# Performance work log

Measured on AMD Instinct MI355X. Metric: run time of the kernel, lower is better.

Reference implementation:

```python
import jax, jax.numpy as jnp
import numpy as np

B, S, H = 2, 2048, 2048
NH, NKV, HD = 16, 4, 128
GROUPS = NH // NKV
THETA = 10000.0
EPS = 1e-6


def setup_inputs() -> dict:
    key = jax.random.key(0)
    ks = jax.random.split(key, 6)
    scale = 0.02
    return {
        "hidden_states": jax.random.normal(ks[0], (B, S, H), jnp.float32),
        "wq": jax.random.normal(ks[1], (NH * HD, H), jnp.float32) * scale,
        "wk": jax.random.normal(ks[2], (NKV * HD, H), jnp.float32) * scale,
        "wv": jax.random.normal(ks[3], (NKV * HD, H), jnp.float32) * scale,
        "wo": jax.random.normal(ks[4], (H, NH * HD), jnp.float32) * scale,
        "q_norm_weight": jnp.ones((HD,), jnp.float32),
        "k_norm_weight": jnp.ones((HD,), jnp.float32),
    }


def _rope_tables(seq_len):
    inv_freq = 1.0 / (THETA ** (jnp.arange(0, HD, 2, dtype=jnp.float32) / HD))
    t = jnp.arange(seq_len, dtype=jnp.float32)
    freqs = jnp.outer(t, inv_freq)              # [S, HD/2]
    emb = jnp.concatenate([freqs, freqs], -1)   # [S, HD]
    return jnp.cos(emb), jnp.sin(emb)


def _rotate_half(x):
    x1, x2 = x[..., : HD // 2], x[..., HD // 2:]
    return jnp.concatenate([-x2, x1], -1)


def _rmsnorm(x, w):
    var = jnp.mean(jnp.square(x), axis=-1, keepdims=True)
    return x * jax.lax.rsqrt(var + EPS) * w


def reference(hidden_states, wq, wk, wv, wo, q_norm_weight, k_norm_weight):
    b, s, _ = hidden_states.shape
    q = (hidden_states @ wq.T).reshape(b, s, NH, HD).transpose(0, 2, 1, 3)    # [b,nh,s,d]
    k = (hidden_states @ wk.T).reshape(b, s, NKV, HD).transpose(0, 2, 1, 3)   # [b,nkv,s,d]
    v = (hidden_states @ wv.T).reshape(b, s, NKV, HD).transpose(0, 2, 1, 3)

    cos, sin = _rope_tables(s)                  # [s,d]
    q = q * cos + _rotate_half(q) * sin
    k = k * cos + _rotate_half(k) * sin

    # fused QK RMSNorm (applied inside fused_qknorm_flash_attention)
    q = _rmsnorm(q, q_norm_weight)
    k = _rmsnorm(k, k_norm_weight)

    # GQA: share each kv head across GROUPS query heads without materializing repeats
    qg = q.reshape(b, NKV, GROUPS, s, HD)
    scale = 1.0 / jnp.sqrt(jnp.float32(HD))
    scores = jnp.einsum('bhgqd,bhkd->bhgqk', qg, k) * scale   # [b,nkv,g,s,s]
    causal = jnp.tril(jnp.ones((s, s), bool))
    scores = jnp.where(causal, scores, jnp.finfo(scores.dtype).min)
    probs = jax.nn.softmax(scores, axis=-1)
    out = jnp.einsum('bhgqk,bhkd->bhgqd', probs, v)            # [b,nkv,g,s,d]
    out = out.reshape(b, NH, s, HD).transpose(0, 2, 1, 3).reshape(b, s, NH * HD)
    return out @ wo.T
```

## Files before the change

### kernel.cpp

```cpp
#include <hip/hip_runtime.h>
#include <math.h>

typedef __bf16 bf16;
typedef __bf16 bf16x8 __attribute__((ext_vector_type(8)));
typedef __bf16 bf16x4 __attribute__((ext_vector_type(4)));
typedef float f32x4 __attribute__((ext_vector_type(4)));

#define B_DIM 2
#define S_LEN 2048
#define H_DIM 2048
#define NH 16
#define NKV 4
#define HD 128

__device__ __forceinline__ void gl_lds16(const void* g, void* l) {
    __builtin_amdgcn_global_load_lds(
        (const __attribute__((address_space(1))) unsigned int*)g,
        (__attribute__((address_space(3))) unsigned int*)l, 16, 0, 0);
}

__global__ __launch_bounds__(256) void cast_all(const float* __restrict__ s0,
                                                const float* __restrict__ s1,
                                                const float* __restrict__ s2,
                                                const float* __restrict__ s3,
                                                const float* __restrict__ s4,
                                                bf16* __restrict__ dst) {
    const int i = blockIdx.x * 256 + threadIdx.x;
    const float* src;
    int off;
    if (i < 2097152)      { src = s0; off = 0; }
    else if (i < 3145728) { src = s1; off = 2097152; }
    else if (i < 3407872) { src = s2; off = 3145728; }
    else if (i < 3670016) { src = s3; off = 3407872; }
    else                  { src = s4; off = 3670016; }
    float4 f = ((const float4*)src)[i - off];
    bf16x4 o = { (bf16)f.x, (bf16)f.y, (bf16)f.z, (bf16)f.w };
    *(bf16x4*)(dst + (size_t)i * 4) = o;
}

template <typename OutT>
__global__ __launch_bounds__(256) void gemm_bt(const bf16* __restrict__ A,
                                               const bf16* __restrict__ Bt,
                                               OutT* __restrict__ C,
                                               int M, int N, int K) {
    __shared__ __align__(16) bf16 As[128 * 32];
    __shared__ __align__(16) bf16 Bs[128 * 32];
    const int t = threadIdx.x;
    const int lane = t & 63, w = t >> 6;
    const int wm = (w & 1) * 64, wn = (w >> 1) * 64;
    const int lr = lane & 15, quad = lane >> 4;
    const int m0 = blockIdx.x * 128, n0 = blockIdx.y * 128;
    const int lrow = lane >> 2, lk = (lane & 3) * 8;
    f32x4 acc[4][4];
#pragma unroll
    for (int i = 0; i < 4; i++)
#pragma unroll
        for (int j = 0; j < 4; j++) acc[i][j] = (f32x4){0.f, 0.f, 0.f, 0.f};

    for (int k0 = 0; k0 < K; k0 += 32) {
        __syncthreads();
#pragma unroll
        for (int i = 0; i < 2; i++) {
            const int r0 = i * 64 + w * 16;
            gl_lds16(A + (size_t)(m0 + r0 + lrow) * K + k0 + lk, &As[r0 * 32]);
            gl_lds16(Bt + (size_t)(n0 + r0 + lrow) * K + k0 + lk, &Bs[r0 * 32]);
        }
        __syncthreads();
        bf16x8 af[4], bfr[4];
#pragma unroll
        for (int i = 0; i < 4; i++) af[i] = *(const bf16x8*)&As[(wm + i * 16 + lr) * 32 + quad * 8];
#pragma unroll
        for (int j = 0; j < 4; j++) bfr[j] = *(const bf16x8*)&Bs[(wn + j * 16 + lr) * 32 + quad * 8];
#pragma unroll
        for (int i = 0; i < 4; i++)
#pragma unroll
            for (int j = 0; j < 4; j++)
                acc[i][j] = __builtin_amdgcn_mfma_f32_16x16x32_bf16(af[i], bfr[j], acc[i][j], 0, 0, 0);
    }
#pragma unroll
    for (int i = 0; i < 4; i++) {
        int m = m0 + wm + i * 16 + quad * 4;
#pragma unroll
        for (int j = 0; j < 4; j++) {
            int n = n0 + wn + j * 16 + lr;
#pragma unroll
            for (int r = 0; r < 4; r++)
                C[(size_t)(m + r) * N + n] = (OutT)acc[i][j][r];
        }
    }
}

__global__ __launch_bounds__(256) void rope_rms(const bf16* __restrict__ qkv,
                                                const float* __restrict__ qw,
                                                const float* __restrict__ kw,
                                                bf16* __restrict__ qb,
                                                bf16* __restrict__ kb,
                                                bf16* __restrict__ vt) {
    const int tok = blockIdx.x;
    const int b = tok >> 11, s = tok & (S_LEN - 1);
    const int lane = threadIdx.x & 63, w = threadIdx.x >> 6;
    const bf16* row = qkv + (size_t)tok * 3072;
    const float inv = expf(-(float)lane * (9.210340371976184f / 64.f));
    const float ang = (float)s * inv;
    float s_, c_;
    sincosf(ang, &s_, &c_);
    const float wq1 = qw[lane], wq2 = qw[lane + 64];
    const float wk1 = kw[lane], wk2 = kw[lane + 64];
    for (int u = w; u < 24; u += 4) {
        if (u < 16) {
            const float x1 = (float)row[u * 128 + lane], x2 = (float)row[u * 128 + 64 + lane];
            float y1 = x1 * c_ - x2 * s_;
            float y2 = x2 * c_ + x1 * s_;
            float ss = y1 * y1 + y2 * y2;
#pragma unroll
            for (int m = 1; m < 64; m <<= 1) ss += __shfl_xor(ss, m);
            const float r = rsqrtf(ss * (1.f / 128.f) + 1e-6f);
            size_t o = ((size_t)(b * NH + u) * S_LEN + s) * HD;
            qb[o + lane]      = (bf16)(y1 * r * wq1);
            qb[o + 64 + lane] = (bf16)(y2 * r * wq2);
        } else if (u < 20) {
            const int kh = u - 16;
            const float x1 = (float)row[2048 + kh * 128 + lane], x2 = (float)row[2048 + kh * 128 + 64 + lane];
            float y1 = x1 * c_ - x2 * s_;
            float y2 = x2 * c_ + x1 * s_;
            float ss = y1 * y1 + y2 * y2;
#pragma unroll
            for (int m = 1; m < 64; m <<= 1) ss += __shfl_xor(ss, m);
            const float r = rsqrtf(ss * (1.f / 128.f) + 1e-6f);
            size_t base = (size_t)(b * NKV + kh) * 16 * 16384;
            kb[base + (size_t)(lane >> 3) * 16384 + s * 8 + (lane & 7)]       = (bf16)(y1 * r * wk1);
            kb[base + (size_t)(8 + (lane >> 3)) * 16384 + s * 8 + (lane & 7)] = (bf16)(y2 * r * wk2);
        } else {
            const int vh = u - 20;
            const float x1 = (float)row[2560 + vh * 128 + lane], x2 = (float)row[2560 + vh * 128 + 64 + lane];
            size_t base = ((size_t)(b * NKV + vh) * 256 + (s >> 3)) * 1024 + (s & 7);
            vt[base + (size_t)lane * 8]        = (bf16)x1;
            vt[base + (size_t)(lane + 64) * 8] = (bf16)x2;
        }
    }
}

__global__ __launch_bounds__(256, 2) void flash(const bf16* __restrict__ qg,
                                                const bf16* __restrict__ kg,
                                                const bf16* __restrict__ vg,
                                                bf16* __restrict__ attn) {
    const int idx = blockIdx.x;
    const int qt = 15 - (idx >> 5);
    const int hb = idx & 31;
    const int h = hb & 15, b = hb >> 4;
    const int kvh = h >> 2;
    const bf16* qh = qg + (size_t)(b * NH + h) * S_LEN * HD;
    const bf16* kh = kg + (size_t)(b * NKV + kvh) * (16 * 16384);
    const bf16* vh = vg + (size_t)(b * NKV + kvh) * (256 * 1024);
    __shared__ __align__(16) bf16 Ks[16 * 512];
    __shared__ __align__(16) bf16 Vs[8 * 1152];
    __shared__ __align__(16) bf16 Ps[4][32 * 72];
    const int t = threadIdx.x, lane = t & 63, w = t >> 6, lr = lane & 15, quad = lane >> 4;
    bf16* psw = Ps[w];
    if (t < 128) {
        const bf16 one = (bf16)1.0f;
        bf16x8 one8 = {one, one, one, one, one, one, one, one};
        *(bf16x8*)&Vs[(t >> 4) * 1152 + 1024 + (t & 15) * 8] = one8;
    }
    const int row0 = qt * 128 + w * 32;
    bf16x8 qf[2][4];
#pragma unroll
    for (int mg = 0; mg < 2; mg++)
#pragma unroll
        for (int c = 0; c < 4; c++)
            qf[mg][c] = *(const bf16x8*)(qh + (size_t)(row0 + mg * 16 + lr) * HD + c * 32 + quad * 8);
    f32x4 o[2][8];
    f32x4 lacc[2];
#pragma unroll
    for (int mg = 0; mg < 2; mg++) {
        lacc[mg] = (f32x4){0.f, 0.f, 0.f, 0.f};
#pragma unroll
        for (int j = 0; j < 8; j++) o[mg][j] = (f32x4){0.f, 0.f, 0.f, 0.f};
    }
    const float C1 = 0.12751744f;
    const float C2 = -17.3123405f;
    const int ntile = 2 * qt + 2;

    for (int kt = 0; kt < ntile; ++kt) {
        const int kbase = kt * 64;
        __syncthreads();
#pragma unroll
        for (int i = 0; i < 4; i++) {
            const int dc = w * 4 + i;
            gl_lds16(kh + (size_t)dc * 16384 + (size_t)kbase * 8 + lane * 8, &Ks[dc * 512]);
        }
#pragma unroll
        for (int i = 0; i < 2; i++) {
            const int c = w * 2 + i;
            const bf16* src = vh + ((size_t)(kbase >> 3) + c) * 1024 + lane * 8;
            gl_lds16(src, &Vs[c * 1152]);
            gl_lds16(src + 512, &Vs[c * 1152 + 512]);
        }
        __syncthreads();
        f32x4 sacc[2][4];
#pragma unroll
        for (int mg = 0; mg < 2; mg++)
#pragma unroll
            for (int n = 0; n < 4; n++) sacc[mg][n] = (f32x4){0.f, 0.f, 0.f, 0.f};
#pragma unroll
        for (int n = 0; n < 4; n++)
#pragma unroll
            for (int c = 0; c < 4; c++) {
                bf16x8 kf = *(const bf16x8*)&Ks[(c * 4 + quad) * 512 + (n * 16 + lr) * 8];
                sacc[0][n] = __builtin_amdgcn_mfma_f32_16x16x32_bf16(qf[0][c], kf, sacc[0][n], 0, 0, 0);
                sacc[1][n] = __builtin_amdgcn_mfma_f32_16x16x32_bf16(qf[1][c], kf, sacc[1][n], 0, 0, 0);
            }
        const bool diag = (kt >= 2 * qt);
#pragma unroll
        for (int mg = 0; mg < 2; mg++)
#pragma unroll
            for (int n = 0; n < 4; n++)
#pragma unroll
                for (int r = 0; r < 4; r++) {
                    float e = exp2f(fmaf(sacc[mg][n][r], C1, C2));
                    if (diag) {
                        const int key = kbase + n * 16 + lr;
                        const int qrow = row0 + mg * 16 + quad * 4 + r;
                        e = (key <= qrow) ? e : 0.f;
                    }
                    psw[(mg * 16 + quad * 4 + r) * 72 + n * 16 + lr] = (bf16)e;
                }
        bf16x8 pf[2][2];
#pragma unroll
        for (int mg = 0; mg < 2; mg++)
#pragma unroll
            for (int k2 = 0; k2 < 2; k2++)
                pf[mg][k2] = *(const bf16x8*)&psw[(mg * 16 + lr) * 72 + k2 * 32 + quad * 8];
#pragma unroll
        for (int k2 = 0; k2 < 2; k2++) {
#pragma unroll
            for (int j = 0; j < 8; j++) {
                bf16x8 vf = *(const bf16x8*)&Vs[(k2 * 4 + quad) * 1152 + (j * 16 + lr) * 8];
                o[0][j] = __builtin_amdgcn_mfma_f32_16x16x32_bf16(pf[0][k2], vf, o[0][j], 0, 0, 0);
                o[1][j] = __builtin_amdgcn_mfma_f32_16x16x32_bf16(pf[1][k2], vf, o[1][j], 0, 0, 0);
            }
            bf16x8 vone = *(const bf16x8*)&Vs[(k2 * 4 + quad) * 1152 + (128 + lr) * 8];
            lacc[0] = __builtin_amdgcn_mfma_f32_16x16x32_bf16(pf[0][k2], vone, lacc[0], 0, 0, 0);
            lacc[1] = __builtin_amdgcn_mfma_f32_16x16x32_bf16(pf[1][k2], vone, lacc[1], 0, 0, 0);
        }
    }
#pragma unroll
    for (int mg = 0; mg < 2; mg++) {
        float inv[4];
#pragma unroll
        for (int r = 0; r < 4; r++) inv[r] = 1.0f / lacc[mg][r];
#pragma unroll
        for (int j = 0; j < 8; j++)
#pragma unroll
            for (int r = 0; r < 4; r++) {
                const int qrow = row0 + mg * 16 + quad * 4 + r;
                attn[((size_t)(b * S_LEN) + qrow) * (NH * HD) + h * HD + j * 16 + lr] =
                    (bf16)(o[mg][j][r] * inv[r]);
            }
    }
}

extern "C" void kernel_launch(void* const* d_in, const int* in_sizes, int n_in,
                              void* d_out, int out_size, void* d_ws, size_t ws_size,
                              hipStream_t stream) {
    (void)in_sizes; (void)n_in; (void)out_size; (void)ws_size;
    const float* hs  = (const float*)d_in[0];
    const float* wq  = (const float*)d_in[1];
    const float* wk  = (const float*)d_in[2];
    const float* wv  = (const float*)d_in[3];
    const float* wo  = (const float*)d_in[4];
    const float* qnw = (const float*)d_in[5];
    const float* knw = (const float*)d_in[6];
    float* out = (float*)d_out;

    char* ws = (char*)d_ws;
    size_t off = 0;
    auto alloc = [&](size_t bytes) {
        void* p = ws + off;
        off += (bytes + 255) & ~(size_t)255;
        return p;
    };
    bf16* hs_bf   = (bf16*)alloc((size_t)4096 * 2048 * 2);
    bf16* wqkv_bf = (bf16*)alloc((size_t)3072 * 2048 * 2);
    bf16* wo_bf   = (bf16*)alloc((size_t)2048 * 2048 * 2);
    bf16* qkv_bf  = (bf16*)alloc((size_t)4096 * 3072 * 2);
    bf16* q_bf    = (bf16*)alloc((size_t)B_DIM * NH * S_LEN * HD * 2);
    bf16* k_bf    = (bf16*)alloc((size_t)B_DIM * NKV * S_LEN * HD * 2);
    bf16* vt_bf   = (bf16*)alloc((size_t)B_DIM * NKV * S_LEN * HD * 2);
    bf16* at_bf   = (bf16*)alloc((size_t)4096 * 2048 * 2);

    cast_all<<<18432, 256, 0, stream>>>(hs, wq, wk, wv, wo, hs_bf);
    gemm_bt<bf16><<<dim3(32, 24), 256, 0, stream>>>(hs_bf, wqkv_bf, qkv_bf, 4096, 3072, 2048);
    rope_rms<<<4096, 256, 0, stream>>>(qkv_bf, qnw, knw, q_bf, k_bf, vt_bf);
    flash<<<dim3(512), 256, 0, stream>>>(q_bf, k_bf, vt_bf, at_bf);
    gemm_bt<float><<<dim3(32, 16), 256, 0, stream>>>(at_bf, wo_bf, out, 4096, 2048, 2048);
}
```

Baseline: 337.9 us.

## Use two waves with 64 query rows each in flash attention

The flash attention block goes from four waves of 32 query rows to two waves of 64 rows, so each wave reuses every K and V fragment loaded from LDS across four MFMA row groups instead of two. This roughly halves LDS read traffic per MFMA. The S accumulation is restructured per key column block to limit live registers. The cost is higher register pressure (larger O accumulators), launch bounds of 128 threads and 1 block, fewer waves per CU for latency hiding, and each thread issuing twice as many global-to-LDS loads.

```diff
diff --git a/kernel.cpp b/kernel.cpp
--- a/kernel.cpp
+++ b/kernel.cpp
@@ -140,7 +140,7 @@
     }
 }
 
-__global__ __launch_bounds__(256, 2) void flash(const bf16* __restrict__ qg,
+__global__ __launch_bounds__(128, 1) void flash(const bf16* __restrict__ qg,
                                                 const bf16* __restrict__ kg,
                                                 const bf16* __restrict__ vg,
                                                 bf16* __restrict__ attn) {
@@ -154,25 +154,25 @@
     const bf16* vh = vg + (size_t)(b * NKV + kvh) * (256 * 1024);
     __shared__ __align__(16) bf16 Ks[16 * 512];
     __shared__ __align__(16) bf16 Vs[8 * 1152];
-    __shared__ __align__(16) bf16 Ps[4][32 * 72];
+    __shared__ __align__(16) bf16 Ps[2][64 * 72];
     const int t = threadIdx.x, lane = t & 63, w = t >> 6, lr = lane & 15, quad = lane >> 4;
     bf16* psw = Ps[w];
-    if (t < 128) {
+    {
         const bf16 one = (bf16)1.0f;
         bf16x8 one8 = {one, one, one, one, one, one, one, one};
         *(bf16x8*)&Vs[(t >> 4) * 1152 + 1024 + (t & 15) * 8] = one8;
     }
-    const int row0 = qt * 128 + w * 32;
-    bf16x8 qf[2][4];
-#pragma unroll
-    for (int mg = 0; mg < 2; mg++)
+    const int row0 = qt * 128 + w * 64;
+    bf16x8 qf[4][4];
+#pragma unroll
+    for (int mg = 0; mg < 4; mg++)
 #pragma unroll
         for (int c = 0; c < 4; c++)
             qf[mg][c] = *(const bf16x8*)(qh + (size_t)(row0 + mg * 16 + lr) * HD + c * 32 + quad * 8);
-    f32x4 o[2][8];
-    f32x4 lacc[2];
-#pragma unroll
-    for (int mg = 0; mg < 2; mg++) {
+    f32x4 o[4][8];
+    f32x4 lacc[4];
+#pragma unroll
+    for (int mg = 0; mg < 4; mg++) {
         lacc[mg] = (f32x4){0.f, 0.f, 0.f, 0.f};
 #pragma unroll
         for (int j = 0; j < 8; j++) o[mg][j] = (f32x4){0.f, 0.f, 0.f, 0.f};
@@ -185,39 +185,37 @@
         const int kbase = kt * 64;
         __syncthreads();
 #pragma unroll
+        for (int i = 0; i < 8; i++) {
+            const int dc = w * 8 + i;
+            gl_lds16(kh + (size_t)dc * 16384 + (size_t)kbase * 8 + lane * 8, &Ks[dc * 512]);
+        }
+#pragma unroll
         for (int i = 0; i < 4; i++) {
-            const int dc = w * 4 + i;
-            gl_lds16(kh + (size_t)dc * 16384 + (size_t)kbase * 8 + lane * 8, &Ks[dc * 512]);
-        }
-#pragma unroll
-        for (int i = 0; i < 2; i++) {
-            const int c = w * 2 + i;
+            const int c = w * 4 + i;
             const bf16* src = vh + ((size_t)(kbase >> 3) + c) * 1024 + lane * 8;
             gl_lds16(src, &Vs[c * 1152]);
             gl_lds16(src + 512, &Vs[c * 1152 + 512]);
         }
         __syncthreads();
-        f32x4 sacc[2][4];
-#pragma unroll
-        for (int mg = 0; mg < 2; mg++)
-#pragma unroll
-            for (int n = 0; n < 4; n++) sacc[mg][n] = (f32x4){0.f, 0.f, 0.f, 0.f};
-#pragma unroll
-        for (int n = 0; n < 4; n++)
+        const bool diag = (kt >= 2 * qt);
+#pragma unroll
+        for (int n = 0; n < 4; n++) {
+            f32x4 sacc[4];
+#pragma unroll
+            for (int mg = 0; mg < 4; mg++) sacc[mg] = (f32x4){0.f, 0.f, 0.f, 0.f};
 #pragma unroll
             for (int c = 0; c < 4; c++) {
                 bf16x8 kf = *(const bf16x8*)&Ks[(c * 4 + quad) * 512 + (n * 16 + lr) * 8];
-                sacc[0][n] = __builtin_amdgcn_mfma_f32_16x16x32_bf16(qf[0][c], kf, sacc[0][n], 0, 0, 0);
-                sacc[1][n] = __builtin_amdgcn_mfma_f32_16x16x32_bf16(qf[1][c], kf, sacc[1][n], 0, 0, 0);
+                sacc[0] = __builtin_amdgcn_mfma_f32_16x16x32_bf16(qf[0][c], kf, sacc[0], 0, 0, 0);
+                sacc[1] = __builtin_amdgcn_mfma_f32_16x16x32_bf16(qf[1][c], kf, sacc[1], 0, 0, 0);
+                sacc[2] = __builtin_amdgcn_mfma_f32_16x16x32_bf16(qf[2][c], kf, sacc[2], 0, 0, 0);
+                sacc[3] = __builtin_amdgcn_mfma_f32_16x16x32_bf16(qf[3][c], kf, sacc[3], 0, 0, 0);
             }
-        const bool diag = (kt >= 2 * qt);
-#pragma unroll
-        for (int mg = 0; mg < 2; mg++)
-#pragma unroll
-            for (int n = 0; n < 4; n++)
+#pragma unroll
+            for (int mg = 0; mg < 4; mg++)
 #pragma unroll
                 for (int r = 0; r < 4; r++) {
-                    float e = exp2f(fmaf(sacc[mg][n][r], C1, C2));
+                    float e = exp2f(fmaf(sacc[mg][r], C1, C2));
                     if (diag) {
                         const int key = kbase + n * 16 + lr;
                         const int qrow = row0 + mg * 16 + quad * 4 + r;
@@ -225,27 +223,29 @@
                     }
                     psw[(mg * 16 + quad * 4 + r) * 72 + n * 16 + lr] = (bf16)e;
                 }
-        bf16x8 pf[2][2];
-#pragma unroll
-        for (int mg = 0; mg < 2; mg++)
-#pragma unroll
-            for (int k2 = 0; k2 < 2; k2++)
-                pf[mg][k2] = *(const bf16x8*)&psw[(mg * 16 + lr) * 72 + k2 * 32 + quad * 8];
+        }
 #pragma unroll
         for (int k2 = 0; k2 < 2; k2++) {
+            bf16x8 pf[4];
+#pragma unroll
+            for (int mg = 0; mg < 4; mg++)
+                pf[mg] = *(const bf16x8*)&psw[(mg * 16 + lr) * 72 + k2 * 32 + quad * 8];
 #pragma unroll
             for (int j = 0; j < 8; j++) {
                 bf16x8 vf = *(const bf16x8*)&Vs[(k2 * 4 + quad) * 1152 + (j * 16 + lr) * 8];
-                o[0][j] = __builtin_amdgcn_mfma_f32_16x16x32_bf16(pf[0][k2], vf, o[0][j], 0, 0, 0);
-                o[1][j] = __builtin_amdgcn_mfma_f32_16x16x32_bf16(pf[1][k2], vf, o[1][j], 0, 0, 0);
+                o[0][j] = __builtin_amdgcn_mfma_f32_16x16x32_bf16(pf[0], vf, o[0][j], 0, 0, 0);
+                o[1][j] = __builtin_amdgcn_mfma_f32_16x16x32_bf16(pf[1], vf, o[1][j], 0, 0, 0);
+                o[2][j] = __builtin_amdgcn_mfma_f32_16x16x32_bf16(pf[2], vf, o[2][j], 0, 0, 0);
+                o[3][j] = __builtin_amdgcn_mfma_f32_16x16x32_bf16(pf[3], vf, o[3][j], 0, 0, 0);
             }
             bf16x8 vone = *(const bf16x8*)&Vs[(k2 * 4 + quad) * 1152 + (128 + lr) * 8];
-            lacc[0] = __builtin_amdgcn_mfma_f32_16x16x32_bf16(pf[0][k2], vone, lacc[0], 0, 0, 0);
-            lacc[1] = __builtin_amdgcn_mfma_f32_16x16x32_bf16(pf[1][k2], vone, lacc[1], 0, 0, 0);
-        }
-    }
-#pragma unroll
-    for (int mg = 0; mg < 2; mg++) {
+#pragma unroll
+            for (int mg = 0; mg < 4; mg++)
+                lacc[mg] = __builtin_amdgcn_mfma_f32_16x16x32_bf16(pf[mg], vone, lacc[mg], 0, 0, 0);
+        }
+    }
+#pragma unroll
+    for (int mg = 0; mg < 4; mg++) {
         float inv[4];
 #pragma unroll
         for (int r = 0; r < 4; r++) inv[r] = 1.0f / lacc[mg][r];
@@ -292,6 +292,6 @@
     cast_all<<<18432, 256, 0, stream>>>(hs, wq, wk, wv, wo, hs_bf);
     gemm_bt<bf16><<<dim3(32, 24), 256, 0, stream>>>(hs_bf, wqkv_bf, qkv_bf, 4096, 3072, 2048);
     rope_rms<<<4096, 256, 0, stream>>>(qkv_bf, qnw, knw, q_bf, k_bf, vt_bf);
-    flash<<<dim3(512), 256, 0, stream>>>(q_bf, k_bf, vt_bf, at_bf);
+    flash<<<dim3(512), 128, 0, stream>>>(q_bf, k_bf, vt_bf, at_bf);
     gemm_bt<float><<<dim3(32, 16), 256, 0, stream>>>(at_bf, wo_bf, out, 4096, 2048, 2048);
 }
```

Result: slower. 412.8 us (+22.2%).
